# Performance work log

Hardware: AMD Instinct MI355X
Metric: run time of the kernel (lower is better)

## Reference

```python
import jax, jax.numpy as jnp
import numpy as np

TAU = 0.5
EPS = 1e-8


def setup_inputs() -> dict:
    key = jax.random.key(0)
    k1, k2 = jax.random.split(key)
    N, D = 16384, 128
    Tx1 = jax.random.normal(k1, (N, D), dtype=jnp.float32)
    Tx2 = jax.random.normal(k2, (N, D), dtype=jnp.float32)
    return {"Tx1": Tx1, "Tx2": Tx2}


def reference(Tx1, Tx2):
    n = Tx1.shape[0]
    # squared pairwise distances ||Tx1_i - Tx2_j||^2 via the expansion trick
    # (matches torch.cdist(...).pow(2), clamped to be non-negative)
    sq1 = jnp.sum(Tx1 * Tx1, axis=1)  # [n]
    sq2 = jnp.sum(Tx2 * Tx2, axis=1)  # [n]
    cross = jnp.einsum('id,jd->ij', Tx1, Tx2)  # [n, n]
    sq_dists = jnp.maximum(sq1[:, None] + sq2[None, :] - 2.0 * cross, 0.0)
    repulsion = jnp.mean(jnp.exp(-sq_dists / (2.0 * TAU)), axis=1)  # [n]
    pos_sq = jnp.sum((Tx1 - Tx2) ** 2, axis=1)  # [n]
    attraction = jnp.exp(-pos_sq / (2.0 * TAU))  # [n]
    loss = jnp.mean(jnp.log1p(repulsion / (attraction + EPS)))
    return loss, jnp.mean(attraction), jnp.mean(repulsion)
```

## Files before the change

### kernel.cpp

```cpp
#include <hip/hip_runtime.h>
#include <hip/hip_bf16.h>


#define EPS 1e-8f
#define D_DIM 128
#define INV_LN2 1.44269504088896f
#define QSCALE 16.0f
#define KQ 0.011271992507f
#define NCHUNK 8
#define TCOLS 64
#define NT 32
#define BM 128

typedef __attribute__((ext_vector_type(4))) int   i32x4;
typedef __attribute__((ext_vector_type(4))) float f32x4;

typedef __attribute__((address_space(1))) const unsigned int gu32_t;
typedef __attribute__((address_space(3))) unsigned int lu32_t;

static __device__ inline void gload_lds16(const void* g, void* l) {
    __builtin_amdgcn_global_load_lds((gu32_t*)g, (lu32_t*)l, 16, 0, 0);
}

static __device__ inline int q8(float x) {
    float r = rintf(x * QSCALE);
    r = fminf(fmaxf(r, -127.f), 127.f);
    return (int)r;
}

static __device__ inline int imax2(int a, int b) { return a > b ? a : b; }

__global__ __launch_bounds__(256) void prep_kernel(
    const float* __restrict__ X1, const float* __restrict__ X2,
    unsigned char* __restrict__ Q1, unsigned char* __restrict__ Q2,
    float* __restrict__ sq1n, float* __restrict__ sq2,
    float* __restrict__ att)
{
    const int w = threadIdx.x >> 6;
    const int l = threadIdx.x & 63;
    const int i = blockIdx.x * 4 + w;
    const float2 a = ((const float2*)(X1 + (size_t)i * D_DIM))[l];
    const float2 b = ((const float2*)(X2 + (size_t)i * D_DIM))[l];

    const int qa0 = q8(a.x), qa1 = q8(a.y);
    const int qb0 = q8(b.x), qb1 = q8(b.y);
    ((ushort*)(Q1 + (size_t)i * D_DIM))[l] =
        (ushort)((qa0 & 0xff) | ((qa1 & 0xff) << 8));
    ((ushort*)(Q2 + (size_t)i * D_DIM))[l] =
        (ushort)((qb0 & 0xff) | ((qb1 & 0xff) << 8));

    float s1 = a.x * a.x + a.y * a.y;
    float s2 = b.x * b.x + b.y * b.y;
    float dx = a.x - b.x, dy = a.y - b.y;
    float ps = dx * dx + dy * dy;
    #pragma unroll
    for (int m = 32; m; m >>= 1) {
        s1 += __shfl_xor(s1, m, 64);
        s2 += __shfl_xor(s2, m, 64);
        ps += __shfl_xor(ps, m, 64);
    }
    if (l == 0) {
        sq1n[i] = -s1 * INV_LN2;
        sq2[i]  =  s2 * INV_LN2;
        att[i]  = __expf(-ps);
    }
}

__global__ __launch_bounds__(512, 4) void cross_kernel(
    const unsigned char* __restrict__ Q1, const unsigned char* __restrict__ Q2,
    const float* __restrict__ sq1n, const float* __restrict__ sq2,
    float* __restrict__ partials, int Ntot)
{
    __shared__ char  bufs[2][8192];
    __shared__ float ldsS1[BM];
    __shared__ float ldsS2[NT * TCOLS];

    const int t    = threadIdx.x;
    const int lane = t & 63;
    const int wid  = t >> 6;
    const int wy   = wid >> 2;
    const int wx   = wid & 3;
    const int lr   = lane & 15;
    const int kg   = lane >> 4;

    const int brow = blockIdx.y * BM;
    const int ccol = blockIdx.x * (NT * TCOLS);

    const char* gA = (const char*)(Q1 + (size_t)brow * D_DIM);
    const char* gB = (const char*)(Q2 + (size_t)ccol * D_DIM);

    #pragma unroll
    for (int it = 0; it < 2; ++it) {
        const unsigned L   = it * 8192u + wid * 1024u + lane * 16u;
        const unsigned src = L ^ (((L >> 7) & 7u) << 4);
        gload_lds16(gA + src, bufs[it] + wid * 1024);
    }
    if (t < BM) ldsS1[t] = sq1n[brow + t];
    ((float4*)ldsS2)[t] = ((const float4*)(sq2 + ccol))[t];
    __syncthreads();

    i32x4 aR[8];
    #pragma unroll
    for (int m = 0; m < 4; ++m) {
        const int lrow = m * 16 + lr;
        #pragma unroll
        for (int kc = 0; kc < 2; ++kc) {
            const unsigned addr = (unsigned)(lrow * 128 + kc * 64 + kg * 16)
                                  ^ (((unsigned)(lrow & 7)) << 4);
            aR[m * 2 + kc] = *(const i32x4*)(bufs[wy] + addr);
        }
    }
    float4 ns1[4];
    #pragma unroll
    for (int m = 0; m < 4; ++m)
        ns1[m] = *(const float4*)(ldsS1 + wy * 64 + m * 16 + kg * 4);
    float thr = -1e30f;
    #pragma unroll
    for (int m = 0; m < 4; ++m)
        thr = fmaxf(thr, fmaxf(fmaxf(ns1[m].x, ns1[m].y),
                               fmaxf(ns1[m].z, ns1[m].w)));
    __syncthreads();

    #pragma unroll
    for (int tile = 0; tile < 2; ++tile) {
        const char* gBt = gB + (size_t)tile * (TCOLS * 128u);
        const unsigned L   = wid * 1024u + lane * 16u;
        const unsigned src = L ^ (((L >> 7) & 7u) << 4);
        gload_lds16(gBt + src, bufs[tile] + wid * 1024);
    }
    asm volatile("s_waitcnt vmcnt(1)" ::: "memory");
    __builtin_amdgcn_s_barrier();
    __builtin_amdgcn_sched_barrier(0);

    float p[4][4];
    #pragma unroll
    for (int m = 0; m < 4; ++m)
        #pragma unroll
        for (int r = 0; r < 4; ++r)
            p[m][r] = 0.f;

    for (int tt = 0; tt < NT; ++tt) {
        char* slot = bufs[tt & 1];

        i32x4 bF[2];
        #pragma unroll
        for (int kc = 0; kc < 2; ++kc) {
            const int row = wx * 16 + lr;
            const unsigned addr = (unsigned)(row * 128 + kc * 64 + kg * 16)
                                  ^ (((unsigned)(row & 7)) << 4);
            bF[kc] = *(const i32x4*)(slot + addr);
        }
        const float s2c = ldsS2[tt * TCOLS + wx * 16 + lr];

        asm volatile("s_waitcnt lgkmcnt(0)" ::: "memory");
        __builtin_amdgcn_sched_barrier(0);
        __builtin_amdgcn_s_barrier();
        __builtin_amdgcn_sched_barrier(0);

        if (tt + 2 < NT) {
            const char* gBn = gB + (size_t)(tt + 2) * (TCOLS * 128u);
            const unsigned L   = wid * 1024u + lane * 16u;
            const unsigned src = L ^ (((L >> 7) & 7u) << 4);
            gload_lds16(gBn + src, slot + wid * 1024);
        }

        i32x4 acc[4];
        #pragma unroll
        for (int m = 0; m < 4; ++m)
            acc[m] = (i32x4){0, 0, 0, 0};

        __builtin_amdgcn_s_setprio(1);
        #pragma unroll
        for (int kc = 0; kc < 2; ++kc)
            #pragma unroll
            for (int m = 0; m < 4; ++m)
                acc[m] = __builtin_amdgcn_mfma_i32_16x16x64_i8(
                    aR[m * 2 + kc], bF[kc], acc[m], 0, 0, 0);
        __builtin_amdgcn_s_setprio(0);

        int ia = imax2(imax2(acc[0][0], acc[0][1]), imax2(acc[0][2], acc[0][3]));
        int ib = imax2(imax2(acc[1][0], acc[1][1]), imax2(acc[1][2], acc[1][3]));
        int ic = imax2(imax2(acc[2][0], acc[2][1]), imax2(acc[2][2], acc[2][3]));
        int id = imax2(imax2(acc[3][0], acc[3][1]), imax2(acc[3][2], acc[3][3]));
        const int imax = imax2(imax2(ia, ib), imax2(ic, id));
        if (__any(fmaf((float)imax, KQ, thr) - s2c > -149.0f)) {
            #pragma unroll
            for (int m = 0; m < 4; ++m)
                #pragma unroll
                for (int r = 0; r < 4; ++r)
                    p[m][r] += __builtin_amdgcn_exp2f(
                        fmaf((float)acc[m][r], KQ,
                             ((const float*)&ns1[m])[r]) - s2c);
        }

        if (tt + 2 < NT) {
            asm volatile("s_waitcnt vmcnt(1)" ::: "memory");
            __builtin_amdgcn_s_barrier();
            __builtin_amdgcn_sched_barrier(0);
        } else if (tt + 1 < NT) {
            asm volatile("s_waitcnt vmcnt(0)" ::: "memory");
            __builtin_amdgcn_s_barrier();
            __builtin_amdgcn_sched_barrier(0);
        }
    }

    const size_t plane = (size_t)(blockIdx.x * 4 + wx) * (size_t)Ntot;
    #pragma unroll
    for (int m = 0; m < 4; ++m) {
        #pragma unroll
        for (int r = 0; r < 4; ++r) {
            float v = p[m][r];
            v += __shfl_xor(v, 1, 64);
            v += __shfl_xor(v, 2, 64);
            v += __shfl_xor(v, 4, 64);
            v += __shfl_xor(v, 8, 64);
            if (lr == 0)
                partials[plane + brow + wy * 64 + m * 16 + kg * 4 + r] = v;
        }
    }
}

__global__ __launch_bounds__(256) void rowsum_kernel(
    const float* __restrict__ partials, const float* __restrict__ att,
    float* __restrict__ blocksums, int N)
{
    __shared__ float sm[3][4];
    const int i = blockIdx.x * 256 + threadIdx.x;
    const float inv = 1.0f / (float)N;
    float s = 0.f;
    #pragma unroll
    for (int pl = 0; pl < 4 * NCHUNK; ++pl)
        s += partials[(size_t)pl * N + i];
    const float rp = s * inv;
    const float at = att[i];
    float ls = log1pf(rp / (at + EPS));
    float sa = at;
    float sr = rp;
    #pragma unroll
    for (int m = 32; m; m >>= 1) {
        ls += __shfl_xor(ls, m, 64);
        sa += __shfl_xor(sa, m, 64);
        sr += __shfl_xor(sr, m, 64);
    }
    const int w = threadIdx.x >> 6, lane = threadIdx.x & 63;
    if (lane == 0) { sm[0][w] = ls; sm[1][w] = sa; sm[2][w] = sr; }
    __syncthreads();
    if (threadIdx.x < 3) {
        const float v = sm[threadIdx.x][0] + sm[threadIdx.x][1]
                      + sm[threadIdx.x][2] + sm[threadIdx.x][3];
        blocksums[threadIdx.x * 64 + blockIdx.x] = v;
    }
}

__global__ __launch_bounds__(192) void final_kernel(
    const float* __restrict__ blocksums, float* __restrict__ out, int N)
{
    const int w = threadIdx.x >> 6;
    const int lane = threadIdx.x & 63;
    float v = blocksums[w * 64 + lane];
    #pragma unroll
    for (int m = 32; m; m >>= 1) v += __shfl_xor(v, m, 64);
    if (lane == 0) out[w] = v / (float)N;
}

extern "C" void kernel_launch(void* const* d_in, const int* in_sizes, int n_in,
                              void* d_out, int out_size, void* d_ws, size_t ws_size,
                              hipStream_t stream)
{
    const float* X1 = (const float*)d_in[0];
    const float* X2 = (const float*)d_in[1];
    const int N = in_sizes[0] / D_DIM;
    float* out = (float*)d_out;

    char* ws = (char*)d_ws;
    unsigned char* Q1 = (unsigned char*)ws;
    unsigned char* Q2 = Q1 + (size_t)N * D_DIM;
    float* sq1n = (float*)(ws + (size_t)2 * N * D_DIM);
    float* sq2 = sq1n + N;
    float* att = sq2 + N;
    float* partials = att + N;
    float* blocksums = partials + (size_t)4 * NCHUNK * N;

    prep_kernel<<<N / 4, 256, 0, stream>>>(X1, X2, Q1, Q2, sq1n, sq2, att);
    dim3 grid(NCHUNK, N / BM);
    cross_kernel<<<grid, 512, 0, stream>>>(Q1, Q2, sq1n, sq2, partials, N);
    rowsum_kernel<<<N / 256, 256, 0, stream>>>(partials, att, blocksums, N);
    final_kernel<<<1, 192, 0, stream>>>(blocksums, out, N);
}
```

Measured before the change: 51.32 us.

## Software-pipeline B-fragment LDS reads with register double buffering, one barrier per tile

The tile loop is manually unrolled by two and alternates between two register sets of B fragments. The next tile's fragments and its s2 values are read from LDS while the current tile's MFMAs and exp accumulation run, and each iteration now has one barrier instead of two. In exchange, the end-of-iteration wait becomes vmcnt(0) instead of vmcnt(1). The global prefetch issued at the start of an iteration must therefore land within that same iteration, which shortens the window for hiding global-load latency.

```diff
diff --git a/kernel.cpp b/kernel.cpp
--- a/kernel.cpp
+++ b/kernel.cpp
@@ -128,7 +128,21 @@
         const unsigned src = L ^ (((L >> 7) & 7u) << 4);
         gload_lds16(gBt + src, bufs[tile] + wid * 1024);
     }
-    asm volatile("s_waitcnt vmcnt(1)" ::: "memory");
+    asm volatile("s_waitcnt vmcnt(0)" ::: "memory");
+    __builtin_amdgcn_s_barrier();
+    __builtin_amdgcn_sched_barrier(0);
+
+    const int  brW   = wx * 16 + lr;
+    const unsigned bAddr0 = (unsigned)(brW * 128 + 0 * 64 + kg * 16)
+                            ^ (((unsigned)(brW & 7)) << 4);
+    const unsigned bAddr1 = (unsigned)(brW * 128 + 1 * 64 + kg * 16)
+                            ^ (((unsigned)(brW & 7)) << 4);
+
+    i32x4 bA0 = *(const i32x4*)(bufs[0] + bAddr0);
+    i32x4 bA1 = *(const i32x4*)(bufs[0] + bAddr1);
+    i32x4 bB0, bB1;
+    float s2c = ldsS2[wx * 16 + lr];
+    asm volatile("s_waitcnt lgkmcnt(0)" ::: "memory");
     __builtin_amdgcn_s_barrier();
     __builtin_amdgcn_sched_barrier(0);
 
@@ -139,70 +153,62 @@
         for (int r = 0; r < 4; ++r)
             p[m][r] = 0.f;
 
-    for (int tt = 0; tt < NT; ++tt) {
-        char* slot = bufs[tt & 1];
-
-        i32x4 bF[2];
-        #pragma unroll
-        for (int kc = 0; kc < 2; ++kc) {
-            const int row = wx * 16 + lr;
-            const unsigned addr = (unsigned)(row * 128 + kc * 64 + kg * 16)
-                                  ^ (((unsigned)(row & 7)) << 4);
-            bF[kc] = *(const i32x4*)(slot + addr);
-        }
-        const float s2c = ldsS2[tt * TCOLS + wx * 16 + lr];
-
-        asm volatile("s_waitcnt lgkmcnt(0)" ::: "memory");
-        __builtin_amdgcn_sched_barrier(0);
-        __builtin_amdgcn_s_barrier();
-        __builtin_amdgcn_sched_barrier(0);
-
-        if (tt + 2 < NT) {
-            const char* gBn = gB + (size_t)(tt + 2) * (TCOLS * 128u);
-            const unsigned L   = wid * 1024u + lane * 16u;
-            const unsigned src = L ^ (((L >> 7) & 7u) << 4);
-            gload_lds16(gBn + src, slot + wid * 1024);
-        }
-
-        i32x4 acc[4];
-        #pragma unroll
-        for (int m = 0; m < 4; ++m)
-            acc[m] = (i32x4){0, 0, 0, 0};
-
-        __builtin_amdgcn_s_setprio(1);
-        #pragma unroll
-        for (int kc = 0; kc < 2; ++kc)
-            #pragma unroll
-            for (int m = 0; m < 4; ++m)
-                acc[m] = __builtin_amdgcn_mfma_i32_16x16x64_i8(
-                    aR[m * 2 + kc], bF[kc], acc[m], 0, 0, 0);
-        __builtin_amdgcn_s_setprio(0);
-
-        int ia = imax2(imax2(acc[0][0], acc[0][1]), imax2(acc[0][2], acc[0][3]));
-        int ib = imax2(imax2(acc[1][0], acc[1][1]), imax2(acc[1][2], acc[1][3]));
-        int ic = imax2(imax2(acc[2][0], acc[2][1]), imax2(acc[2][2], acc[2][3]));
-        int id = imax2(imax2(acc[3][0], acc[3][1]), imax2(acc[3][2], acc[3][3]));
-        const int imax = imax2(imax2(ia, ib), imax2(ic, id));
-        if (__any(fmaf((float)imax, KQ, thr) - s2c > -149.0f)) {
-            #pragma unroll
-            for (int m = 0; m < 4; ++m)
-                #pragma unroll
-                for (int r = 0; r < 4; ++r)
-                    p[m][r] += __builtin_amdgcn_exp2f(
-                        fmaf((float)acc[m][r], KQ,
-                             ((const float*)&ns1[m])[r]) - s2c);
-        }
-
-        if (tt + 2 < NT) {
-            asm volatile("s_waitcnt vmcnt(1)" ::: "memory");
-            __builtin_amdgcn_s_barrier();
-            __builtin_amdgcn_sched_barrier(0);
-        } else if (tt + 1 < NT) {
-            asm volatile("s_waitcnt vmcnt(0)" ::: "memory");
-            __builtin_amdgcn_s_barrier();
-            __builtin_amdgcn_sched_barrier(0);
-        }
-    }
+#define CROSS_ITER(TT, BC0, BC1, BN0, BN1)                                   \
+    {                                                                        \
+        const int tc = (TT);                                                 \
+        if (tc + 2 < NT) {                                                   \
+            const char* gBn = gB + (size_t)(tc + 2) * (TCOLS * 128u);        \
+            const unsigned L   = wid * 1024u + lane * 16u;                   \
+            const unsigned src = L ^ (((L >> 7) & 7u) << 4);                 \
+            gload_lds16(gBn + src, bufs[tc & 1] + wid * 1024);               \
+        }                                                                    \
+        float s2n = s2c;                                                     \
+        if (tc + 1 < NT) {                                                   \
+            BN0 = *(const i32x4*)(bufs[(tc + 1) & 1] + bAddr0);              \
+            BN1 = *(const i32x4*)(bufs[(tc + 1) & 1] + bAddr1);              \
+            s2n = ldsS2[(tc + 1) * TCOLS + wx * 16 + lr];                    \
+        }                                                                    \
+        i32x4 acc[4];                                                        \
+        _Pragma("unroll")                                                    \
+        for (int m = 0; m < 4; ++m) acc[m] = (i32x4){0, 0, 0, 0};            \
+        __builtin_amdgcn_s_setprio(1);                                       \
+        _Pragma("unroll")                                                    \
+        for (int m = 0; m < 4; ++m)                                          \
+            acc[m] = __builtin_amdgcn_mfma_i32_16x16x64_i8(                  \
+                aR[m * 2 + 0], BC0, acc[m], 0, 0, 0);                        \
+        _Pragma("unroll")                                                    \
+        for (int m = 0; m < 4; ++m)                                          \
+            acc[m] = __builtin_amdgcn_mfma_i32_16x16x64_i8(                  \
+                aR[m * 2 + 1], BC1, acc[m], 0, 0, 0);                        \
+        __builtin_amdgcn_s_setprio(0);                                       \
+        int ia = imax2(imax2(acc[0][0], acc[0][1]), imax2(acc[0][2], acc[0][3])); \
+        int ib = imax2(imax2(acc[1][0], acc[1][1]), imax2(acc[1][2], acc[1][3])); \
+        int ic = imax2(imax2(acc[2][0], acc[2][1]), imax2(acc[2][2], acc[2][3])); \
+        int id = imax2(imax2(acc[3][0], acc[3][1]), imax2(acc[3][2], acc[3][3])); \
+        const int imax = imax2(imax2(ia, ib), imax2(ic, id));                \
+        if (__any(fmaf((float)imax, KQ, thr) - s2c > -149.0f)) {             \
+            _Pragma("unroll")                                                \
+            for (int m = 0; m < 4; ++m)                                      \
+                _Pragma("unroll")                                            \
+                for (int r = 0; r < 4; ++r)                                  \
+                    p[m][r] += __builtin_amdgcn_exp2f(                       \
+                        fmaf((float)acc[m][r], KQ,                           \
+                             ((const float*)&ns1[m])[r]) - s2c);             \
+        }                                                                    \
+        s2c = s2n;                                                           \
+        if (tc + 1 < NT) {                                                   \
+            asm volatile("s_waitcnt lgkmcnt(0)" ::: "memory");               \
+            asm volatile("s_waitcnt vmcnt(0)" ::: "memory");                 \
+            __builtin_amdgcn_s_barrier();                                    \
+            __builtin_amdgcn_sched_barrier(0);                               \
+        }                                                                    \
+    }
+
+    for (int tp = 0; tp < NT; tp += 2) {
+        CROSS_ITER(tp,     bA0, bA1, bB0, bB1);
+        CROSS_ITER(tp + 1, bB0, bB1, bA0, bA1);
+    }
+#undef CROSS_ITER
 
     const size_t plane = (size_t)(blockIdx.x * 4 + wx) * (size_t)Ntot;
     #pragma unroll
```

Measured after the change: 54.51 us. +6.2%, slower.

## Process two B tiles per barrier phase with four-slot LDS ring

Applied to the files above, without the earlier changes.

The cross-product loop now handles two column tiles per iteration, using a four-buffer LDS ring with prefetch of the next pair of tiles. This halves the number of block-wide barriers and waitcnt stalls, and gives the scheduler two independent MFMA accumulator chains to interleave. In exchange it doubles the LDS used for B tiles (32 KB instead of 16 KB) and raises register pressure from the second accumulator set, which could reduce occupancy at four blocks per CU.

```diff
diff --git a/kernel.cpp b/kernel.cpp
--- a/kernel.cpp
+++ b/kernel.cpp
@@ -10,6 +10,7 @@
 #define NCHUNK 8
 #define TCOLS 64
 #define NT 32
+#define NPH 16
 #define BM 128
 
 typedef __attribute__((ext_vector_type(4))) int   i32x4;
@@ -71,7 +72,7 @@
     const float* __restrict__ sq1n, const float* __restrict__ sq2,
     float* __restrict__ partials, int Ntot)
 {
-    __shared__ char  bufs[2][8192];
+    __shared__ char  bufs[4][8192];
     __shared__ float ldsS1[BM];
     __shared__ float ldsS2[NT * TCOLS];
 
@@ -122,16 +123,22 @@
     __syncthreads();
 
     #pragma unroll
-    for (int tile = 0; tile < 2; ++tile) {
+    for (int tile = 0; tile < 4; ++tile) {
         const char* gBt = gB + (size_t)tile * (TCOLS * 128u);
         const unsigned L   = wid * 1024u + lane * 16u;
         const unsigned src = L ^ (((L >> 7) & 7u) << 4);
         gload_lds16(gBt + src, bufs[tile] + wid * 1024);
     }
-    asm volatile("s_waitcnt vmcnt(1)" ::: "memory");
+    asm volatile("s_waitcnt vmcnt(2)" ::: "memory");
     __builtin_amdgcn_s_barrier();
     __builtin_amdgcn_sched_barrier(0);
 
+    const int  brW   = wx * 16 + lr;
+    const unsigned bAddr0 = (unsigned)(brW * 128 + 0 * 64 + kg * 16)
+                            ^ (((unsigned)(brW & 7)) << 4);
+    const unsigned bAddr1 = (unsigned)(brW * 128 + 1 * 64 + kg * 16)
+                            ^ (((unsigned)(brW & 7)) << 4);
+
     float p[4][4];
     #pragma unroll
     for (int m = 0; m < 4; ++m)
@@ -139,70 +146,91 @@
         for (int r = 0; r < 4; ++r)
             p[m][r] = 0.f;
 
-    for (int tt = 0; tt < NT; ++tt) {
-        char* slot = bufs[tt & 1];
-
-        i32x4 bF[2];
-        #pragma unroll
-        for (int kc = 0; kc < 2; ++kc) {
-            const int row = wx * 16 + lr;
-            const unsigned addr = (unsigned)(row * 128 + kc * 64 + kg * 16)
-                                  ^ (((unsigned)(row & 7)) << 4);
-            bF[kc] = *(const i32x4*)(slot + addr);
-        }
-        const float s2c = ldsS2[tt * TCOLS + wx * 16 + lr];
+#define EPILOG(ACC, S2)                                                      \
+    {                                                                        \
+        int ia = imax2(imax2(ACC[0][0], ACC[0][1]), imax2(ACC[0][2], ACC[0][3])); \
+        int ib = imax2(imax2(ACC[1][0], ACC[1][1]), imax2(ACC[1][2], ACC[1][3])); \
+        int ic = imax2(imax2(ACC[2][0], ACC[2][1]), imax2(ACC[2][2], ACC[2][3])); \
+        int id = imax2(imax2(ACC[3][0], ACC[3][1]), imax2(ACC[3][2], ACC[3][3])); \
+        const int imx = imax2(imax2(ia, ib), imax2(ic, id));                 \
+        if (__any(fmaf((float)imx, KQ, thr) - (S2) > -149.0f)) {             \
+            _Pragma("unroll")                                                \
+            for (int m = 0; m < 4; ++m)                                      \
+                _Pragma("unroll")                                            \
+                for (int r = 0; r < 4; ++r)                                  \
+                    p[m][r] += __builtin_amdgcn_exp2f(                       \
+                        fmaf((float)ACC[m][r], KQ,                           \
+                             ((const float*)&ns1[m])[r]) - (S2));            \
+        }                                                                    \
+    }
+
+    for (int k = 0; k < NPH; ++k) {
+        char* slotE = bufs[(k & 1) * 2 + 0];
+        char* slotO = bufs[(k & 1) * 2 + 1];
+
+        i32x4 bE0 = *(const i32x4*)(slotE + bAddr0);
+        i32x4 bE1 = *(const i32x4*)(slotE + bAddr1);
+        i32x4 bO0 = *(const i32x4*)(slotO + bAddr0);
+        i32x4 bO1 = *(const i32x4*)(slotO + bAddr1);
+        const float s2E = ldsS2[(2 * k)     * TCOLS + wx * 16 + lr];
+        const float s2O = ldsS2[(2 * k + 1) * TCOLS + wx * 16 + lr];
 
         asm volatile("s_waitcnt lgkmcnt(0)" ::: "memory");
         __builtin_amdgcn_sched_barrier(0);
         __builtin_amdgcn_s_barrier();
         __builtin_amdgcn_sched_barrier(0);
 
-        if (tt + 2 < NT) {
-            const char* gBn = gB + (size_t)(tt + 2) * (TCOLS * 128u);
-            const unsigned L   = wid * 1024u + lane * 16u;
-            const unsigned src = L ^ (((L >> 7) & 7u) << 4);
-            gload_lds16(gBn + src, slot + wid * 1024);
+        if (k + 1 < NPH) {
+            #pragma unroll
+            for (int half = 0; half < 2; ++half) {
+                const int tile = 2 * (k + 2) + half;
+                if (tile < NT) {
+                    const char* gBn = gB + (size_t)tile * (TCOLS * 128u);
+                    const unsigned L   = wid * 1024u + lane * 16u;
+                    const unsigned src = L ^ (((L >> 7) & 7u) << 4);
+                    gload_lds16(gBn + src,
+                                ((half == 0) ? slotE : slotO) + wid * 1024);
+                }
+            }
         }
 
-        i32x4 acc[4];
+        i32x4 accE[4], accO[4];
+        #pragma unroll
+        for (int m = 0; m < 4; ++m) { accE[m] = (i32x4){0,0,0,0};
+                                      accO[m] = (i32x4){0,0,0,0}; }
+        __builtin_amdgcn_s_setprio(1);
         #pragma unroll
         for (int m = 0; m < 4; ++m)
-            acc[m] = (i32x4){0, 0, 0, 0};
-
-        __builtin_amdgcn_s_setprio(1);
-        #pragma unroll
-        for (int kc = 0; kc < 2; ++kc)
-            #pragma unroll
-            for (int m = 0; m < 4; ++m)
-                acc[m] = __builtin_amdgcn_mfma_i32_16x16x64_i8(
-                    aR[m * 2 + kc], bF[kc], acc[m], 0, 0, 0);
+            accE[m] = __builtin_amdgcn_mfma_i32_16x16x64_i8(
+                aR[m * 2 + 0], bE0, accE[m], 0, 0, 0);
+        #pragma unroll
+        for (int m = 0; m < 4; ++m)
+            accE[m] = __builtin_amdgcn_mfma_i32_16x16x64_i8(
+                aR[m * 2 + 1], bE1, accE[m], 0, 0, 0);
+        #pragma unroll
+        for (int m = 0; m < 4; ++m)
+            accO[m] = __builtin_amdgcn_mfma_i32_16x16x64_i8(
+                aR[m * 2 + 0], bO0, accO[m], 0, 0, 0);
+        #pragma unroll
+        for (int m = 0; m < 4; ++m)
+            accO[m] = __builtin_amdgcn_mfma_i32_16x16x64_i8(
+                aR[m * 2 + 1], bO1, accO[m], 0, 0, 0);
         __builtin_amdgcn_s_setprio(0);
 
-        int ia = imax2(imax2(acc[0][0], acc[0][1]), imax2(acc[0][2], acc[0][3]));
-        int ib = imax2(imax2(acc[1][0], acc[1][1]), imax2(acc[1][2], acc[1][3]));
-        int ic = imax2(imax2(acc[2][0], acc[2][1]), imax2(acc[2][2], acc[2][3]));
-        int id = imax2(imax2(acc[3][0], acc[3][1]), imax2(acc[3][2], acc[3][3]));
-        const int imax = imax2(imax2(ia, ib), imax2(ic, id));
-        if (__any(fmaf((float)imax, KQ, thr) - s2c > -149.0f)) {
-            #pragma unroll
-            for (int m = 0; m < 4; ++m)
-                #pragma unroll
-                for (int r = 0; r < 4; ++r)
-                    p[m][r] += __builtin_amdgcn_exp2f(
-                        fmaf((float)acc[m][r], KQ,
-                             ((const float*)&ns1[m])[r]) - s2c);
-        }
-
-        if (tt + 2 < NT) {
-            asm volatile("s_waitcnt vmcnt(1)" ::: "memory");
-            __builtin_amdgcn_s_barrier();
-            __builtin_amdgcn_sched_barrier(0);
-        } else if (tt + 1 < NT) {
-            asm volatile("s_waitcnt vmcnt(0)" ::: "memory");
+        EPILOG(accE, s2E);
+        EPILOG(accO, s2O);
+
+        if (k + 1 < NPH) {
+            if (k + 2 < NPH) {
+                asm volatile("s_waitcnt vmcnt(2)" ::: "memory");
+            } else {
+                asm volatile("s_waitcnt vmcnt(0)" ::: "memory");
+            }
             __builtin_amdgcn_s_barrier();
             __builtin_amdgcn_sched_barrier(0);
         }
     }
+#undef EPILOG
 
     const size_t plane = (size_t)(blockIdx.x * 4 + wx) * (size_t)Ntot;
     #pragma unroll
```

Result: no change. 50.43 us (-1.7%).
